# Performance work log

Measured on AMD Instinct MI355X. Metric: run time of the kernel, lower is better.

Reference implementation:

```python
import jax, jax.numpy as jnp
import numpy as np
import itertools

# ---- static configuration (matches init_kwargs) ----
LS = [0, 1, 2, 3]            # spherical harmonic degrees, parity (-1)^l
MUL = 128                    # channel multiplicity of hklm / output
N_EDGES = 16384
DIMS = [2 * l + 1 for l in LS]
Y_DIM = sum(DIMS)                        # 16
H_DIM = sum(d * MUL for d in DIMS)       # 2048
Y_OFF = np.cumsum([0] + DIMS).tolist()
H_OFF = np.cumsum([0] + [d * MUL for d in DIMS]).tolist()

# ---- real-basis O(3) Clebsch-Gordan coefficients (numpy, setup-time) ----
def _su2_generators(l):
    m = np.arange(-l, l + 1)
    Lz = np.diag(m).astype(np.complex128)
    vals = np.sqrt(l * (l + 1) - m[:-1] * (m[:-1] + 1))
    Lp = np.zeros((2 * l + 1, 2 * l + 1), np.complex128)
    Lp[np.arange(1, 2 * l + 1), np.arange(2 * l)] = vals
    Lm = Lp.T.copy()
    return (Lp + Lm) / 2.0, (Lp - Lm) / 2.0j, Lz

def _c2r(l):
    # unitary change of basis: complex SH -> real SH
    d = 2 * l + 1
    U = np.zeros((d, d), np.complex128)
    U[l, l] = 1.0
    s2 = 1.0 / np.sqrt(2.0)
    for m in range(1, l + 1):
        U[l + m, l + m] = (-1) ** m * s2
        U[l + m, l - m] = s2
        U[l - m, l + m] = -1j * (-1) ** m * s2
        U[l - m, l - m] = 1j * s2
    return U

def _real_generators(l):
    U = _c2r(l)
    return [np.real(-1j * (U @ L @ U.conj().T)) for L in _su2_generators(l)]

def _cg(l1, l2, l3):
    # invariant tensor = null space of the summed infinitesimal rotation action
    G1, G2, G3 = _real_generators(l1), _real_generators(l2), _real_generators(l3)
    d1, d2, d3 = 2 * l1 + 1, 2 * l2 + 1, 2 * l3 + 1
    I1, I2, I3 = np.eye(d1), np.eye(d2), np.eye(d3)
    rows = []
    for k in range(3):
        rows.append(np.kron(np.kron(G1[k], I2), I3)
                    + np.kron(np.kron(I1, G2[k]), I3)
                    + np.kron(np.kron(I1, I2), G3[k]))
    K = np.concatenate(rows, axis=0)
    _, s, Vt = np.linalg.svd(K)
    c = Vt[-1].reshape(d1, d2, d3)
    c = c / np.linalg.norm(c)
    c = c * np.sign(c.reshape(-1)[np.argmax(np.abs(c))])  # deterministic sign
    return c

PATHS = []
_CG_LIST = []
for (i1, l1), (i2, l2), (i3, l3) in itertools.product(enumerate(LS), enumerate(LS), enumerate(LS)):
    # triangle inequality + O3 parity selection rule ((-1)^l parities)
    if abs(l1 - l2) <= l3 <= l1 + l2 and (l1 + l2 + l3) % 2 == 0:
        PATHS.append((i1, i2, i3))
        _CG_LIST.append(_cg(l1, l2, l3))
N_PATHS = len(PATHS)                    # 23
W_DIM = N_PATHS * MUL                   # 2944
CG_OFF = np.cumsum([0] + [c.size for c in _CG_LIST]).tolist()
CGC_NP = np.concatenate([c.reshape(-1) for c in _CG_LIST]).astype(np.float32)


def setup_inputs() -> dict:
    key = jax.random.key(0)
    k1, k2, k3 = jax.random.split(key, 3)
    return {
        "Ylm": jax.random.normal(k1, (N_EDGES, Y_DIM), jnp.float32),
        "hklm": jax.random.normal(k2, (N_EDGES, H_DIM), jnp.float32),
        "weight": jax.random.normal(k3, (N_EDGES, W_DIM), jnp.float32),
        "CGC": jnp.asarray(CGC_NP),   # registered buffer in the torch module
    }


def reference(Ylm, hklm, weight, CGC):
    # segmented tensor product 'abcu,a,bu,cu' with per-path weight fused in:
    # out[n, c, u] += sum_{a,b} CG_p[a,b,c] * w_p[n,u] * Y[n,a] * h[n,b,u]
    N = Ylm.shape[0]
    out = jnp.zeros((N, H_DIM), Ylm.dtype)
    for p, (i1, i2, i3) in enumerate(PATHS):
        d1, d2, d3 = DIMS[i1], DIMS[i2], DIMS[i3]
        cg = CGC[CG_OFF[p]:CG_OFF[p + 1]].reshape(d1, d2, d3)
        y = Ylm[:, Y_OFF[i1]:Y_OFF[i1] + d1]
        h = hklm[:, H_OFF[i2]:H_OFF[i2] + d2 * MUL].reshape(N, d2, MUL)
        w = weight[:, p * MUL:(p + 1) * MUL]
        z = jnp.einsum('abc,na,nbu->ncu', cg, y, h) * w[:, None, :]
        out = out.at[:, H_OFF[i3]:H_OFF[i3] + d3 * MUL].add(z.reshape(N, d3 * MUL))
    return out
```

## Files before the change

### kernel.cpp

```cpp
#include <hip/hip_runtime.h>


#define BS 256
#define EPB 2
#define TPE 128
#define YD 16
#define HD 2048
#define WD 2944
#define NP 23
#define BTOT 484

typedef float f4 __attribute__((ext_vector_type(4)));

__host__ __device__ constexpr int coff(int l) {
  return l == 0 ? 0 : (l == 1 ? 1 : (l == 2 ? 4 : 9));
}

#define FOR_PATHS(X) \
  X(0, 0,0,0,    0,   0) \
  X(1, 0,1,1,    1,  24) \
  X(2, 0,2,2,   10, 108) \
  X(3, 0,3,3,   35, 276) \
  X(4, 1,0,1,   84,   4) \
  X(5, 1,1,0,   93,  36) \
  X(6, 1,1,2,  102,  40) \
  X(7, 1,2,1,  147, 136) \
  X(8, 1,2,3,  192, 152) \
  X(9, 1,3,2,  297, 328) \
  X(10,2,0,2,  402,   8) \
  X(11,2,1,1,  427,  56) \
  X(12,2,1,3,  472,  68) \
  X(13,2,2,0,  577, 188) \
  X(14,2,2,2,  602, 196) \
  X(15,2,3,1,  727, 364) \
  X(16,2,3,3,  832, 388) \
  X(17,3,0,3, 1077,  16) \
  X(18,3,1,2, 1126,  92) \
  X(19,3,2,1, 1231, 224) \
  X(20,3,2,3, 1336, 240) \
  X(21,3,3,0, 1581, 440) \
  X(22,3,3,2, 1630, 448)

template <int D2, int D3, int BO, int C3>
__device__ __forceinline__ void dopath(const float* __restrict__ Bg,
                                       const float* __restrict__ hh,
                                       float wv, float (&acc)[YD]) {
  float s[D3];
#pragma unroll
  for (int m3 = 0; m3 < D3; ++m3) s[m3] = 0.f;
  f4 c;
#pragma unroll
  for (int f = 0; f < D2 * D3; ++f) {
    if ((f & 3) == 0) c = *(const f4*)(Bg + BO + f);
    s[f / D2] += c[f & 3] * hh[f % D2];
  }
#pragma unroll
  for (int m3 = 0; m3 < D3; ++m3) acc[C3 + m3] += s[m3] * wv;
}

__global__ __launch_bounds__(BS, 6) void etp_kernel(
    const float* __restrict__ Y, const float* __restrict__ H,
    const float* __restrict__ W, const float* __restrict__ CG,
    float* __restrict__ O) {
  const int g = threadIdx.x >> 7;
  const int u = threadIdx.x & 127;
  const size_t n = (size_t)blockIdx.x * EPB + g;

  __shared__ __align__(16) float Bsm[EPB][BTOT];
  __shared__ float ysm[EPB][YD];

  { const int t = threadIdx.x;
    if (t < EPB * YD) {
      const int e = t >> 4, c = t & 15;
      ysm[e][c] = Y[(size_t)(blockIdx.x * EPB + e) * YD + c];
    } }
  __syncthreads();

#define BUILD(P, L1, L2, L3, CGO, BO) { \
    constexpr int d1 = 2*(L1)+1, d2 = 2*(L2)+1, d3 = 2*(L3)+1; \
    if (u < d2 * d3) { \
      const int m3 = u / d2, m2 = u - m3 * d2; \
      float s = 0.f; \
      _Pragma("unroll") \
      for (int a = 0; a < d1; ++a) \
        s += CG[(CGO) + (a * d2 + m2) * d3 + m3] * ysm[g][coff(L1) + a]; \
      Bsm[g][(BO) + u] = s; \
    } }
  FOR_PATHS(BUILD)
#undef BUILD
  __syncthreads();

  const float* __restrict__ Hn = H + n * HD + u;
  const float* __restrict__ Wn = W + n * WD + u;
  float* __restrict__ On = O + n * HD + u;
  const float* __restrict__ Bg = &Bsm[g][0];

  float h[YD];
#pragma unroll
  for (int c = 0; c < YD; ++c) h[c] = Hn[c * TPE];
  float w[NP];
#pragma unroll
  for (int p = 0; p < NP; ++p) w[p] = Wn[p * TPE];
#pragma unroll
  for (int c = 0; c < YD; ++c) asm volatile("" : "+v"(h[c]));
#pragma unroll
  for (int p = 0; p < NP; ++p) asm volatile("" : "+v"(w[p]));

  float acc[YD];
#pragma unroll
  for (int c = 0; c < YD; ++c) acc[c] = 0.f;

#define DOP(P, L1, L2, L3, CGO, BO) \
  dopath<2*(L2)+1, 2*(L3)+1, BO, coff(L3)>(Bg, &h[coff(L2)], w[P], acc);
  FOR_PATHS(DOP)
#undef DOP

#pragma unroll
  for (int c = 0; c < YD; ++c)
    __builtin_nontemporal_store(acc[c], &On[c * TPE]);
}

extern "C" void kernel_launch(void* const* d_in, const int* in_sizes, int n_in,
                              void* d_out, int out_size, void* d_ws, size_t ws_size,
                              hipStream_t stream) {
  const float* Y  = (const float*)d_in[0];
  const float* H  = (const float*)d_in[1];
  const float* W  = (const float*)d_in[2];
  const float* CG = (const float*)d_in[3];
  float* O = (float*)d_out;

  const int n_edges = in_sizes[0] / YD;
  etp_kernel<<<n_edges / EPB, BS, 0, stream>>>(Y, H, W, CG, O);
}
```

Baseline: 97.70 us.

## Process two channels per thread to reuse LDS coefficients across channels

Each thread now handles channels u and u+64 of one edge, with one wavefront per edge and four edges per block. Every coefficient vector read from LDS is reused for two channel FMAs, halving LDS traffic per unit of math. Weight loads are grouped by input degree so that fewer weight registers are live at once. The cost is more live registers per thread (two h and two acc arrays), so launch bounds drop from 6 to 4 blocks, which may reduce latency hiding in a kernel that is largely bandwidth-bound.

```diff
diff --git a/kernel.cpp b/kernel.cpp
--- a/kernel.cpp
+++ b/kernel.cpp
@@ -2,12 +2,10 @@
 
 
 #define BS 256
-#define EPB 2
-#define TPE 128
+#define EPB 4
 #define YD 16
 #define HD 2048
 #define WD 2944
-#define NP 23
 #define BTOT 484
 
 typedef float f4 __attribute__((ext_vector_type(4)));
@@ -43,27 +41,34 @@
 
 template <int D2, int D3, int BO, int C3>
 __device__ __forceinline__ void dopath(const float* __restrict__ Bg,
-                                       const float* __restrict__ hh,
-                                       float wv, float (&acc)[YD]) {
-  float s[D3];
-#pragma unroll
-  for (int m3 = 0; m3 < D3; ++m3) s[m3] = 0.f;
+                                       const float* __restrict__ h0,
+                                       const float* __restrict__ h1,
+                                       float wv0, float wv1,
+                                       float (&acc0)[YD], float (&acc1)[YD]) {
+  float s0[D3], s1[D3];
+#pragma unroll
+  for (int m3 = 0; m3 < D3; ++m3) { s0[m3] = 0.f; s1[m3] = 0.f; }
   f4 c;
 #pragma unroll
   for (int f = 0; f < D2 * D3; ++f) {
     if ((f & 3) == 0) c = *(const f4*)(Bg + BO + f);
-    s[f / D2] += c[f & 3] * hh[f % D2];
-  }
-#pragma unroll
-  for (int m3 = 0; m3 < D3; ++m3) acc[C3 + m3] += s[m3] * wv;
-}
-
-__global__ __launch_bounds__(BS, 6) void etp_kernel(
+    const float b = c[f & 3];
+    s0[f / D2] += b * h0[f % D2];
+    s1[f / D2] += b * h1[f % D2];
+  }
+#pragma unroll
+  for (int m3 = 0; m3 < D3; ++m3) {
+    acc0[C3 + m3] += s0[m3] * wv0;
+    acc1[C3 + m3] += s1[m3] * wv1;
+  }
+}
+
+__global__ __launch_bounds__(BS, 4) void etp_kernel(
     const float* __restrict__ Y, const float* __restrict__ H,
     const float* __restrict__ W, const float* __restrict__ CG,
     float* __restrict__ O) {
-  const int g = threadIdx.x >> 7;
-  const int u = threadIdx.x & 127;
+  const int g = threadIdx.x >> 6;
+  const int l = threadIdx.x & 63;
   const size_t n = (size_t)blockIdx.x * EPB + g;
 
   __shared__ __align__(16) float Bsm[EPB][BTOT];
@@ -78,46 +83,107 @@
 
 #define BUILD(P, L1, L2, L3, CGO, BO) { \
     constexpr int d1 = 2*(L1)+1, d2 = 2*(L2)+1, d3 = 2*(L3)+1; \
-    if (u < d2 * d3) { \
-      const int m3 = u / d2, m2 = u - m3 * d2; \
+    if (l < d2 * d3) { \
+      const int m3 = l / d2, m2 = l - m3 * d2; \
       float s = 0.f; \
       _Pragma("unroll") \
       for (int a = 0; a < d1; ++a) \
         s += CG[(CGO) + (a * d2 + m2) * d3 + m3] * ysm[g][coff(L1) + a]; \
-      Bsm[g][(BO) + u] = s; \
+      Bsm[g][(BO) + l] = s; \
     } }
   FOR_PATHS(BUILD)
 #undef BUILD
   __syncthreads();
 
-  const float* __restrict__ Hn = H + n * HD + u;
-  const float* __restrict__ Wn = W + n * WD + u;
-  float* __restrict__ On = O + n * HD + u;
+  const float* __restrict__ Hn = H + n * HD + l;
+  const float* __restrict__ Wn = W + n * WD + l;
+  float* __restrict__ On = O + n * HD + l;
   const float* __restrict__ Bg = &Bsm[g][0];
 
-  float h[YD];
-#pragma unroll
-  for (int c = 0; c < YD; ++c) h[c] = Hn[c * TPE];
-  float w[NP];
-#pragma unroll
-  for (int p = 0; p < NP; ++p) w[p] = Wn[p * TPE];
-#pragma unroll
-  for (int c = 0; c < YD; ++c) asm volatile("" : "+v"(h[c]));
-#pragma unroll
-  for (int p = 0; p < NP; ++p) asm volatile("" : "+v"(w[p]));
-
-  float acc[YD];
-#pragma unroll
-  for (int c = 0; c < YD; ++c) acc[c] = 0.f;
-
-#define DOP(P, L1, L2, L3, CGO, BO) \
-  dopath<2*(L2)+1, 2*(L3)+1, BO, coff(L3)>(Bg, &h[coff(L2)], w[P], acc);
-  FOR_PATHS(DOP)
+  float h0[YD], h1[YD];
+#pragma unroll
+  for (int c = 0; c < YD; ++c) {
+    h0[c] = Hn[c * 128];
+    h1[c] = Hn[c * 128 + 64];
+  }
+#pragma unroll
+  for (int c = 0; c < YD; ++c) {
+    asm volatile("" : "+v"(h0[c]));
+    asm volatile("" : "+v"(h1[c]));
+  }
+
+  float acc0[YD], acc1[YD];
+#pragma unroll
+  for (int c = 0; c < YD; ++c) { acc0[c] = 0.f; acc1[c] = 0.f; }
+
+#define DOP(P, L2, L3, BO, WI) \
+  dopath<2*(L2)+1, 2*(L3)+1, BO, coff(L3)>(Bg, &h0[coff(L2)], &h1[coff(L2)], \
+                                           wg0[WI], wg1[WI], acc0, acc1);
+
+  {
+    float wg0[4], wg1[4];
+    const int pid[4] = {0, 4, 10, 17};
+#pragma unroll
+    for (int i = 0; i < 4; ++i) {
+      wg0[i] = Wn[pid[i] * 128]; wg1[i] = Wn[pid[i] * 128 + 64];
+    }
+#pragma unroll
+    for (int i = 0; i < 4; ++i) {
+      asm volatile("" : "+v"(wg0[i])); asm volatile("" : "+v"(wg1[i]));
+    }
+    DOP(0, 0, 0, 0, 0)  DOP(4, 0, 1, 4, 1)
+    DOP(10, 0, 2, 8, 2) DOP(17, 0, 3, 16, 3)
+  }
+  {
+    float wg0[6], wg1[6];
+    const int pid[6] = {1, 5, 6, 11, 12, 18};
+#pragma unroll
+    for (int i = 0; i < 6; ++i) {
+      wg0[i] = Wn[pid[i] * 128]; wg1[i] = Wn[pid[i] * 128 + 64];
+    }
+#pragma unroll
+    for (int i = 0; i < 6; ++i) {
+      asm volatile("" : "+v"(wg0[i])); asm volatile("" : "+v"(wg1[i]));
+    }
+    DOP(1, 1, 1, 24, 0)   DOP(5, 1, 0, 36, 1)  DOP(6, 1, 2, 40, 2)
+    DOP(11, 1, 1, 56, 3)  DOP(12, 1, 3, 68, 4) DOP(18, 1, 2, 92, 5)
+  }
+  {
+    float wg0[7], wg1[7];
+    const int pid[7] = {2, 7, 8, 13, 14, 19, 20};
+#pragma unroll
+    for (int i = 0; i < 7; ++i) {
+      wg0[i] = Wn[pid[i] * 128]; wg1[i] = Wn[pid[i] * 128 + 64];
+    }
+#pragma unroll
+    for (int i = 0; i < 7; ++i) {
+      asm volatile("" : "+v"(wg0[i])); asm volatile("" : "+v"(wg1[i]));
+    }
+    DOP(2, 2, 2, 108, 0)   DOP(7, 2, 1, 136, 1)  DOP(8, 2, 3, 152, 2)
+    DOP(13, 2, 0, 188, 3)  DOP(14, 2, 2, 196, 4) DOP(19, 2, 1, 224, 5)
+    DOP(20, 2, 3, 240, 6)
+  }
+  {
+    float wg0[6], wg1[6];
+    const int pid[6] = {3, 9, 15, 16, 21, 22};
+#pragma unroll
+    for (int i = 0; i < 6; ++i) {
+      wg0[i] = Wn[pid[i] * 128]; wg1[i] = Wn[pid[i] * 128 + 64];
+    }
+#pragma unroll
+    for (int i = 0; i < 6; ++i) {
+      asm volatile("" : "+v"(wg0[i])); asm volatile("" : "+v"(wg1[i]));
+    }
+    DOP(3, 3, 3, 276, 0)   DOP(9, 3, 2, 328, 1)  DOP(15, 3, 1, 364, 2)
+    DOP(16, 3, 3, 388, 3)  DOP(21, 3, 0, 440, 4) DOP(22, 3, 2, 448, 5)
+  }
 #undef DOP
 
 #pragma unroll
-  for (int c = 0; c < YD; ++c)
-    __builtin_nontemporal_store(acc[c], &On[c * TPE]);
+  for (int c = 0; c < YD; ++c) {
+    __builtin_nontemporal_store(acc0[c], &On[c * 128]);
+    __builtin_nontemporal_store(acc1[c], &On[c * 128 + 64]);
+  }
 }
 
 extern "C" void kernel_launch(void* const* d_in, const int* in_sizes, int n_in,
```

Result: slower. 192.1 us (+96.6%).
